# Kernel tuning notes

Hardware: AMD Instinct MI355X
Metric: run time of the kernel (lower is better)

## Reference

```python
import jax, jax.numpy as jnp
import numpy as np

B, T, D_IN, D, KS = 8, 2048, 64, 512, 3
N_LAYERS = 6
TOP_P = 0.25


def _causal_conv(x, w, b, dil):
    # x: [B, C_in, T], w: [C_out, C_in, K] -> [B, C_out, T]
    pad = (w.shape[-1] - 1) * dil
    y = jax.lax.conv_general_dilated(
        x, w, window_strides=(1,), padding=[(pad, 0)], rhs_dilation=(dil,),
        dimension_numbers=('NCH', 'OIH', 'NCH'))
    return y + b[None, :, None]


def setup_inputs() -> dict:
    key = jax.random.key(0)
    ks = jax.random.split(key, 20)
    s = 0.02
    inp = {
        'x': jax.random.normal(ks[0], (B, T, D_IN), jnp.float32),
        # block 0 (d_in=64 -> d_model=512, dilation 1) + 1x1 residual
        'c1w0': jax.random.normal(ks[1], (D, D_IN, KS), jnp.float32) * s,
        'c1b0': jnp.zeros((D,), jnp.float32),
        'c2w0': jax.random.normal(ks[2], (D, D, KS), jnp.float32) * s,
        'c2b0': jnp.zeros((D,), jnp.float32),
        'resw': jax.random.normal(ks[3], (D, D_IN, 1), jnp.float32) * s,
        'resb': jnp.zeros((D,), jnp.float32),
        # blocks 1..5 stacked (512 -> 512, dilations 2,4,8,16,32), identity residual
        'c1w': jax.random.normal(ks[4], (N_LAYERS - 1, D, D, KS), jnp.float32) * s,
        'c1b': jnp.zeros((N_LAYERS - 1, D), jnp.float32),
        'c2w': jax.random.normal(ks[5], (N_LAYERS - 1, D, D, KS), jnp.float32) * s,
        'c2b': jnp.zeros((N_LAYERS - 1, D), jnp.float32),
        # attention projections (torch Linear: y = x @ W.T + b, W [out,in])
        'wq': jax.random.normal(ks[6], (D, D), jnp.float32) * s,
        'bq': jnp.zeros((D,), jnp.float32),
        'wk': jax.random.normal(ks[7], (D, D), jnp.float32) * s,
        'bk': jnp.zeros((D,), jnp.float32),
        'wv': jax.random.normal(ks[8], (D, D), jnp.float32) * s,
        'bv': jnp.zeros((D,), jnp.float32),
        'wp': jax.random.normal(ks[9], (D, D), jnp.float32) * s,
        'bp': jnp.zeros((D,), jnp.float32),
    }
    return inp


def _forward(x, c1w0, c1b0, c2w0, c2b0, resw, resb, c1w, c1b, c2w, c2b,
             wq, bq, wk, bk, wv, bv, wp, bp):
    gelu = lambda t: jax.nn.gelu(t, approximate=False)
    h = jnp.swapaxes(x, 1, 2)  # [B, D_IN, T]
    # block 0 with 1x1-conv residual (d_in != d_out)
    y = gelu(_causal_conv(h, c1w0, c1b0, 1))
    y = gelu(_causal_conv(y, c2w0, c2b0, 1))
    h = y + _causal_conv(h, resw, resb, 1)
    # blocks 1..5, identity residual
    for i in range(N_LAYERS - 1):
        dil = 2 ** (i + 1)
        y = gelu(_causal_conv(h, c1w[i], c1b[i], dil))
        y = gelu(_causal_conv(y, c2w[i], c2b[i], dil))
        h = y + h
    z = jnp.swapaxes(h, 1, 2)  # [B, T, D]

    # sparse top-p attention
    q = z @ wq.T + bq
    k = z @ wk.T + bk
    v = z @ wv.T + bv
    scores = jnp.einsum('bqd,bkd->bqk', q, k) / jnp.sqrt(jnp.float32(D))
    k_keep = max(1, int(TOP_P * T))
    vals, idx = jax.lax.top_k(scores, k_keep)  # [B, T, k_keep]
    neg_inf = jnp.array(-jnp.inf, scores.dtype)
    mask = jnp.full_like(scores, neg_inf)
    b_ix = jnp.arange(B)[:, None, None]
    t_ix = jnp.arange(T)[None, :, None]
    mask = mask.at[b_ix, t_ix, idx].set(vals)
    attn = jax.nn.softmax(mask, axis=-1)
    attn_out = jnp.einsum('bqk,bkd->bqd', attn, v)[:, -1, :]  # [B, D]

    return (z[:, -1, :] + attn_out) @ wp.T + bp


def reference(x, c1w0, c1b0, c2w0, c2b0, resw, resb, c1w, c1b, c2w, c2b,
              wq, bq, wk, bk, wv, bv, wp, bp):
    return _forward(x, c1w0, c1b0, c2w0, c2b0, resw, resb, c1w, c1b, c2w, c2b,
                    wq, bq, wk, bk, wv, bv, wp, bp)
```

## Files before the change

### kernel.cpp

```cpp
#include <hip/hip_runtime.h>
#include <hip/hip_bf16.h>
#include <math.h>

#define B_ 8
#define T_ 2048
#define PT_ 2112
#define DIN_ 64
#define D_ 512

typedef __attribute__((ext_vector_type(8))) short bf16x8;
typedef __attribute__((ext_vector_type(4))) float f32x4;

#define HROW(b, t) (((size_t)(b) * PT_ + 64 + (t)) * D_)

__device__ __forceinline__ float gelu_f(float x) {
    return 0.5f * x * (1.0f + erff(x * 0.70710678118654752440f));
}
__device__ __forceinline__ float bfu2f(unsigned short u) {
    union { float f; unsigned int i; } v; v.i = ((unsigned int)u) << 16; return v.f;
}
__device__ __forceinline__ unsigned short f2bf(float f) {
    unsigned int x = __float_as_uint(f);
    return (unsigned short)((x + 0x7FFFu + ((x >> 16) & 1u)) >> 16);
}
__device__ __forceinline__ void gload_lds16(const void* g, void* l) {
    __builtin_amdgcn_global_load_lds(
        (const __attribute__((address_space(1))) void*)g,
        (__attribute__((address_space(3))) void*)l, 16, 0, 0);
}

__global__ __launch_bounds__(256) void k_zeropad(unsigned short* xb,
                                                 unsigned short* bufA,
                                                 unsigned short* bufB) {
    const int NX = B_ * 64 * DIN_;
    const int NA = B_ * 64 * D_;
    int i = blockIdx.x * 256 + threadIdx.x;
    if (i < NX) {
        const int b = i / (64 * DIN_), r = i - b * (64 * DIN_);
        xb[(size_t)b * PT_ * DIN_ + r] = 0;
        return;
    }
    i -= NX;
    if (i < NA) {
        const int b = i / (64 * D_), r = i - b * (64 * D_);
        bufA[(size_t)b * PT_ * D_ + r] = 0;
        return;
    }
    i -= NA;
    if (i < NA) {
        const int b = i / (64 * D_), r = i - b * (64 * D_);
        bufB[(size_t)b * PT_ * D_ + r] = 0;
    }
}

__global__ __launch_bounds__(256) void k_xcvt(const float* __restrict__ x,
                                              unsigned short* __restrict__ xb, int n) {
    const int i = blockIdx.x * 256 + threadIdx.x;
    if (i >= n) return;
    const int b = i / (T_ * DIN_);
    const int r = i - b * (T_ * DIN_);
    xb[((size_t)b * PT_ + 64) * DIN_ + r] = f2bf(x[i]);
}

__global__ __launch_bounds__(256) void k_wcvt(const float* __restrict__ src,
                                              unsigned short* __restrict__ dst,
                                              int C_in, int KS) {
    const int n = 512 * C_in * KS;
    const size_t base = (size_t)blockIdx.y * n;
    for (int i = blockIdx.x * 256 + threadIdx.x; i < n; i += gridDim.x * 256) {
        const int ci = i % C_in;
        const int r = i / C_in;
        const int co = r & 511;
        const int tap = r >> 9;
        dst[base + i] = f2bf(src[base + ((size_t)co * C_in + ci) * KS + tap]);
    }
}

template <int KS, int MODE>
__global__ __launch_bounds__(256, 2) void k_conv_mfma(const unsigned short* __restrict__ X,
                                                      const unsigned short* __restrict__ Wt,
                                                      const float* __restrict__ bias,
                                                      const unsigned short* R,
                                                      unsigned short* Y,
                                                      int C_in, int dil) {
    const int tid = threadIdx.x;
    const int t0 = blockIdx.x * 128;
    const int co0 = blockIdx.y * 128;
    const int b = blockIdx.z;
    const int back = (KS - 1) * dil;

    __shared__ __align__(16) unsigned short sX[2][192 * 64];
    __shared__ __align__(16) unsigned short sW[2][128 * 64];

    const int lane = tid & 63;
    const int wv = tid >> 6;
    const int wco = (wv & 1) * 64;
    const int wt = (wv >> 1) * 64;
    const int tl = lane & 15;
    const int ch = lane >> 4;

    f32x4 acc[4][4] = {};

    const unsigned short* Xb = X + ((size_t)b * PT_ + 64) * C_in;

    const unsigned short* xsrc[6];
#pragma unroll
    for (int k = 0; k < 6; ++k) {
        const int i = tid + k * 256;
        const int row = i >> 3, s = i & 7;
        int tg = t0 - back + row;
        if (tg >= T_) tg = T_ - 1;
        xsrc[k] = Xb + (size_t)tg * C_in + ((s ^ (row & 7)) << 3);
    }
    const unsigned short* wsrc[4];
#pragma unroll
    for (int k = 0; k < 4; ++k) {
        const int i = tid + k * 256;
        const int row = i >> 3, s = i & 7;
        wsrc[k] = Wt + (size_t)(co0 + row) * C_in + ((s ^ (row & 7)) << 3);
    }
    const size_t tapstride = (size_t)512 * C_in;

    auto stageX = [&](int c) {
        unsigned short* dst = sX[c & 1];
#pragma unroll
        for (int k = 0; k < 6; ++k) {
            const int i = tid + k * 256;
            gload_lds16(xsrc[k] + c * 64, &dst[(i & ~63) * 8]);
        }
    };
    auto stageW = [&](int c, int tap, int buf) {
        unsigned short* dst = sW[buf];
#pragma unroll
        for (int k = 0; k < 4; ++k) {
            const int i = tid + k * 256;
            gload_lds16(wsrc[k] + (size_t)tap * tapstride + c * 64, &dst[(i & ~63) * 8]);
        }
    };
    auto phase_reads = [&](int pp, int cb, int tap, bf16x8 (&a)[2][4], bf16x8 (&bb)[2][4]) {
        const unsigned short* bW = sW[pp];
        const unsigned short* bX = sX[cb];
        const int tapoff = tap * dil;
#pragma unroll
        for (int ks = 0; ks < 2; ++ks) {
            const int j = ks * 4 + ch;
#pragma unroll
            for (int m = 0; m < 4; ++m) {
                const int wr = wco + m * 16 + tl;
                a[ks][m] = *reinterpret_cast<const bf16x8*>(&bW[wr * 64 + ((j ^ (wr & 7)) << 3)]);
            }
#pragma unroll
            for (int n = 0; n < 4; ++n) {
                const int xr = wt + n * 16 + tl + tapoff;
                bb[ks][n] = *reinterpret_cast<const bf16x8*>(&bX[xr * 64 + ((j ^ (xr & 7)) << 3)]);
            }
        }
    };
    auto domfma = [&](bf16x8 (&a)[2][4], bf16x8 (&bb)[2][4]) {
        __builtin_amdgcn_s_setprio(1);
#pragma unroll
        for (int ks = 0; ks < 2; ++ks)
#pragma unroll
            for (int m = 0; m < 4; ++m)
#pragma unroll
                for (int n = 0; n < 4; ++n)
                    acc[m][n] = __builtin_amdgcn_mfma_f32_16x16x32_bf16(a[ks][m], bb[ks][n], acc[m][n], 0, 0, 0);
        __builtin_amdgcn_s_setprio(0);
    };

    if constexpr (KS == 1) {
        stageX(0);
        stageW(0, 0, 0);
        __syncthreads();
        bf16x8 a[2][4], bb[2][4];
        phase_reads(0, 0, 0, a, bb);
        domfma(a, bb);
    } else {
        const int NC = C_in >> 6;
        const int NPH = NC * 3;
        stageX(0);
        stageW(0, 0, 0);
        stageW(0, 1, 1);
        asm volatile("s_waitcnt vmcnt(4)" ::: "memory");
        __builtin_amdgcn_sched_barrier(0);
        __builtin_amdgcn_s_barrier();

        int c = 0, t = 0;
        for (int ph = 0; ph + 3 < NPH; ++ph) {
            bf16x8 a[2][4], bb[2][4];
            phase_reads(ph & 1, c & 1, t, a, bb);
            asm volatile("s_waitcnt lgkmcnt(0)" ::: "memory");
            __builtin_amdgcn_sched_barrier(0);
            __builtin_amdgcn_s_barrier();
            int t2 = t + 2, c2 = c;
            if (t2 >= 3) { t2 -= 3; ++c2; }
            stageW(c2, t2, ph & 1);
            if (t == 0) stageX(c + 1);
            domfma(a, bb);
            if (t < 2) { asm volatile("s_waitcnt vmcnt(10)" ::: "memory"); }
            else       { asm volatile("s_waitcnt vmcnt(4)"  ::: "memory"); }
            __builtin_amdgcn_sched_barrier(0);
            __builtin_amdgcn_s_barrier();
            if (++t == 3) { t = 0; ++c; }
        }
        {
            bf16x8 a[2][4], bb[2][4];
            phase_reads((NPH - 3) & 1, (NC - 1) & 1, 0, a, bb);
            asm volatile("s_waitcnt lgkmcnt(0)" ::: "memory");
            __builtin_amdgcn_sched_barrier(0);
            __builtin_amdgcn_s_barrier();
            stageW(NC - 1, 2, (NPH - 3) & 1);
            domfma(a, bb);
            asm volatile("s_waitcnt vmcnt(4)" ::: "memory");
            __builtin_amdgcn_sched_barrier(0);
            __builtin_amdgcn_s_barrier();
        }
        {
            bf16x8 a[2][4], bb[2][4];
            phase_reads((NPH - 2) & 1, (NC - 1) & 1, 1, a, bb);
            asm volatile("s_waitcnt lgkmcnt(0)" ::: "memory");
            __builtin_amdgcn_sched_barrier(0);
            __builtin_amdgcn_s_barrier();
            domfma(a, bb);
            asm volatile("s_waitcnt vmcnt(0)" ::: "memory");
            __builtin_amdgcn_sched_barrier(0);
            __builtin_amdgcn_s_barrier();
        }
        {
            bf16x8 a[2][4], bb[2][4];
            phase_reads((NPH - 1) & 1, (NC - 1) & 1, 2, a, bb);
            domfma(a, bb);
        }
    }

#pragma unroll
    for (int m = 0; m < 4; ++m) {
        const int co = co0 + wco + m * 16 + ch * 4;
        const float4 bv4 = *reinterpret_cast<const float4*>(&bias[co]);
#pragma unroll
        for (int n = 0; n < 4; ++n) {
            const int t = t0 + wt + n * 16 + tl;
            const size_t base = HROW(b, t) + co;
            float v[4];
            v[0] = acc[m][n][0] + bv4.x;
            v[1] = acc[m][n][1] + bv4.y;
            v[2] = acc[m][n][2] + bv4.z;
            v[3] = acc[m][n][3] + bv4.w;
            if (MODE >= 1) {
#pragma unroll
                for (int r = 0; r < 4; ++r) v[r] = gelu_f(v[r]);
            }
            if (MODE == 2) {
                const uint2 rr = *reinterpret_cast<const uint2*>(&R[base]);
                v[0] += bfu2f((unsigned short)(rr.x & 0xffffu));
                v[1] += bfu2f((unsigned short)(rr.x >> 16));
                v[2] += bfu2f((unsigned short)(rr.y & 0xffffu));
                v[3] += bfu2f((unsigned short)(rr.y >> 16));
            }
            uint2 o;
            o.x = (unsigned int)f2bf(v[0]) | ((unsigned int)f2bf(v[1]) << 16);
            o.y = (unsigned int)f2bf(v[2]) | ((unsigned int)f2bf(v[3]) << 16);
            *reinterpret_cast<uint2*>(&Y[base]) = o;
        }
    }
}

__global__ __launch_bounds__(256) void k_q(const unsigned short* __restrict__ h,
                                           const float* __restrict__ wq,
                                           const float* __restrict__ bq,
                                           float* __restrict__ q) {
    __shared__ float zs[B_ * D_];
    const int tid = threadIdx.x;
    for (int i = tid; i < B_ * D_; i += 256) {
        const int b = i >> 9, c = i & 511;
        zs[i] = bfu2f(h[HROW(b, T_ - 1) + c]);
    }
    __syncthreads();
    const int wvi = tid >> 6, lane = tid & 63;
    const int d = blockIdx.x * 4 + wvi;
    const float* wr = wq + (size_t)d * D_ + lane * 8;
    float w8[8];
#pragma unroll
    for (int j = 0; j < 8; ++j) w8[j] = wr[j];
    float acc[B_];
#pragma unroll
    for (int b = 0; b < B_; ++b) {
        float a = 0.0f;
#pragma unroll
        for (int j = 0; j < 8; ++j) a += w8[j] * zs[b * D_ + lane * 8 + j];
        acc[b] = a;
    }
#pragma unroll
    for (int off = 32; off; off >>= 1) {
#pragma unroll
        for (int b = 0; b < B_; ++b) acc[b] += __shfl_xor(acc[b], off);
    }
    if (lane == 0) {
#pragma unroll
        for (int b = 0; b < B_; ++b) q[b * D_ + d] = acc[b] + bq[d];
    }
}

__global__ __launch_bounds__(512) void k_qk(const float* __restrict__ q,
                                            const float* __restrict__ wk,
                                            const float* __restrict__ bk,
                                            float* __restrict__ qkvec,
                                            float* __restrict__ qbk) {
    const int b = blockIdx.y, dc = blockIdx.x;
    const int tid = threadIdx.x;
    __shared__ float qs[64];
    if (tid < 64) qs[tid] = q[b * D_ + dc * 64 + tid];
    __syncthreads();
    float acc = 0.0f;
    const float* wbase = wk + (size_t)(dc * 64) * D_ + tid;
#pragma unroll 8
    for (int d = 0; d < 64; ++d) acc += qs[d] * wbase[(size_t)d * D_];
    atomicAdd(&qkvec[b * D_ + tid], acc);
    if (tid < 64) {
        float p = qs[tid] * bk[dc * 64 + tid];
#pragma unroll
        for (int off = 32; off; off >>= 1) p += __shfl_xor(p, off);
        if (tid == 0) atomicAdd(&qbk[b], p);
    }
}

__global__ __launch_bounds__(256) void k_scores(const unsigned short* __restrict__ h,
                                                const float* __restrict__ qkvec,
                                                const float* __restrict__ qbk,
                                                float* __restrict__ scores) {
    const int b = blockIdx.y;
    const int tid = threadIdx.x;
    __shared__ float qs[D_];
    qs[tid] = qkvec[b * D_ + tid];
    qs[tid + 256] = qkvec[b * D_ + tid + 256];
    __syncthreads();
    const int wvi = tid >> 6, lane = tid & 63;
    const int t = blockIdx.x * 4 + wvi;
    const uint4 v = *reinterpret_cast<const uint4*>(h + HROW(b, t) + lane * 8);
    const unsigned int w[4] = {v.x, v.y, v.z, v.w};
    float acc = 0.0f;
#pragma unroll
    for (int j = 0; j < 4; ++j) {
        acc += bfu2f((unsigned short)(w[j] & 0xffffu)) * qs[lane * 8 + 2 * j];
        acc += bfu2f((unsigned short)(w[j] >> 16)) * qs[lane * 8 + 2 * j + 1];
    }
    for (int off = 32; off; off >>= 1) acc += __shfl_down(acc, off);
    if (lane == 0) scores[b * T_ + t] = (acc + qbk[b]) * 0.04419417382415922f;
}

__global__ __launch_bounds__(1024) void k_topk(const float* __restrict__ scores,
                                               float* __restrict__ wts) {
    const int b = blockIdx.x;
    __shared__ float s[T_];
    __shared__ float v[T_];
    __shared__ float red[16];
    __shared__ float denom_s;
    for (int i = threadIdx.x; i < T_; i += 1024) {
        const float x = scores[b * T_ + i];
        s[i] = x; v[i] = x;
    }
    __syncthreads();
    for (unsigned kk = 2; kk <= T_; kk <<= 1) {
        for (unsigned j = kk >> 1; j > 0; j >>= 1) {
            for (unsigned i = threadIdx.x; i < T_; i += 1024) {
                const unsigned ixj = i ^ j;
                if (ixj > i) {
                    const float a = v[i], c2 = v[ixj];
                    const bool asc = ((i & kk) == 0);
                    if ((a > c2) == asc) { v[i] = c2; v[ixj] = a; }
                }
            }
            __syncthreads();
        }
    }
    const float thr = v[T_ - 512];
    const float mx = v[T_ - 1];
    float part = 0.0f;
    for (int i = threadIdx.x; i < T_; i += 1024) {
        const float x = s[i];
        if (x >= thr) part += expf(x - mx);
    }
    for (int off = 32; off; off >>= 1) part += __shfl_down(part, off);
    const int lane = threadIdx.x & 63, wv_ = threadIdx.x >> 6;
    if (lane == 0) red[wv_] = part;
    __syncthreads();
    if (threadIdx.x == 0) {
        float d = 0.0f;
        for (int i = 0; i < 16; ++i) d += red[i];
        denom_s = d;
    }
    __syncthreads();
    const float inv = 1.0f / denom_s;
    for (int i = threadIdx.x; i < T_; i += 1024) {
        const float x = s[i];
        wts[b * T_ + i] = (x >= thr) ? expf(x - mx) * inv : 0.0f;
    }
}

__global__ __launch_bounds__(256) void k_zv(const unsigned short* __restrict__ h,
                                            const float* __restrict__ wts,
                                            float* __restrict__ zvb) {
    const int b = blockIdx.y;
    const int t0 = blockIdx.x * 256;
    const int tid = threadIdx.x;
    float a0 = 0.0f, a1 = 0.0f;
    for (int t = t0; t < t0 + 256; ++t) {
        const float w = wts[b * T_ + t];
        if (w != 0.0f) {
            const unsigned int v = *reinterpret_cast<const unsigned int*>(
                h + HROW(b, t) + tid * 2);
            a0 += w * bfu2f((unsigned short)(v & 0xffffu));
            a1 += w * bfu2f((unsigned short)(v >> 16));
        }
    }
    atomicAdd(&zvb[b * D_ + tid * 2], a0);
    atomicAdd(&zvb[b * D_ + tid * 2 + 1], a1);
}

__global__ __launch_bounds__(256) void k_u(const unsigned short* __restrict__ h,
                                           const float* __restrict__ zvb,
                                           const float* __restrict__ wv,
                                           const float* __restrict__ bv,
                                           float* __restrict__ u) {
    __shared__ float zs[B_ * D_];
    const int tid = threadIdx.x;
    for (int i = tid; i < B_ * D_; i += 256) zs[i] = zvb[i];
    __syncthreads();
    const int wvi = tid >> 6, lane = tid & 63;
    const int e = blockIdx.x * 4 + wvi;
    const float* wr = wv + (size_t)e * D_ + lane * 8;
    float w8[8];
#pragma unroll
    for (int j = 0; j < 8; ++j) w8[j] = wr[j];
    float acc[B_];
#pragma unroll
    for (int b = 0; b < B_; ++b) {
        float a = 0.0f;
#pragma unroll
        for (int j = 0; j < 8; ++j) a += w8[j] * zs[b * D_ + lane * 8 + j];
        acc[b] = a;
    }
#pragma unroll
    for (int off = 32; off; off >>= 1) {
#pragma unroll
        for (int b = 0; b < B_; ++b) acc[b] += __shfl_xor(acc[b], off);
    }
    if (lane == 0) {
#pragma unroll
        for (int b = 0; b < B_; ++b)
            u[b * D_ + e] = acc[b] + bv[e] + bfu2f(h[HROW(b, T_ - 1) + e]);
    }
}

__global__ __launch_bounds__(256) void k_out(const float* __restrict__ u,
                                             const float* __restrict__ wp,
                                             const float* __restrict__ bp,
                                             float* __restrict__ out) {
    __shared__ float us[B_ * D_];
    const int tid = threadIdx.x;
    for (int i = tid; i < B_ * D_; i += 256) us[i] = u[i];
    __syncthreads();
    const int wvi = tid >> 6, lane = tid & 63;
    const int d = blockIdx.x * 4 + wvi;
    const float* wr = wp + (size_t)d * D_ + lane * 8;
    float w8[8];
#pragma unroll
    for (int j = 0; j < 8; ++j) w8[j] = wr[j];
    float acc[B_];
#pragma unroll
    for (int b = 0; b < B_; ++b) {
        float a = 0.0f;
#pragma unroll
        for (int j = 0; j < 8; ++j) a += w8[j] * us[b * D_ + lane * 8 + j];
        acc[b] = a;
    }
#pragma unroll
    for (int off = 32; off; off >>= 1) {
#pragma unroll
        for (int b = 0; b < B_; ++b) acc[b] += __shfl_xor(acc[b], off);
    }
    if (lane == 0) {
#pragma unroll
        for (int b = 0; b < B_; ++b) out[b * D_ + d] = acc[b] + bp[d];
    }
}

extern "C" void kernel_launch(void* const* d_in, const int* in_sizes, int n_in,
                              void* d_out, int out_size, void* d_ws, size_t ws_size,
                              hipStream_t stream) {
    const float* x    = (const float*)d_in[0];
    const float* c1w0 = (const float*)d_in[1];
    const float* c1b0 = (const float*)d_in[2];
    const float* c2w0 = (const float*)d_in[3];
    const float* c2b0 = (const float*)d_in[4];
    const float* resw = (const float*)d_in[5];
    const float* resb = (const float*)d_in[6];
    const float* c1w  = (const float*)d_in[7];
    const float* c1b  = (const float*)d_in[8];
    const float* c2w  = (const float*)d_in[9];
    const float* c2b  = (const float*)d_in[10];
    const float* wq   = (const float*)d_in[11];
    const float* bq   = (const float*)d_in[12];
    const float* wk   = (const float*)d_in[13];
    const float* bk   = (const float*)d_in[14];
    const float* wvp  = (const float*)d_in[15];
    const float* bv   = (const float*)d_in[16];
    const float* wp   = (const float*)d_in[17];
    const float* bp   = (const float*)d_in[18];
    float* out = (float*)d_out;

    unsigned short* ws16 = (unsigned short*)d_ws;
    unsigned short* xb   = ws16;
    unsigned short* bufA = xb + (size_t)B_ * PT_ * DIN_;
    unsigned short* bufB = bufA + (size_t)B_ * PT_ * D_;
    unsigned short* wRes = bufB + (size_t)B_ * PT_ * D_;
    unsigned short* wC10 = wRes + 512 * 64;
    unsigned short* wC20 = wC10 + 3 * 512 * 64;
    unsigned short* wC1  = wC20 + 3 * 512 * 512;
    unsigned short* wC2  = wC1 + (size_t)5 * 3 * 512 * 512;
    float* fws  = (float*)(wC2 + (size_t)5 * 3 * 512 * 512);
    float* qv    = fws;
    float* qkvec = qv + B_ * D_;
    float* qbk   = qkvec + B_ * D_;
    float* zvb   = qbk + 8;
    float* uacc  = zvb + B_ * D_;
    float* sc    = uacc + B_ * D_;
    float* wts   = sc + B_ * T_;

    k_zeropad<<<dim3((B_ * 64 * (DIN_ + 2 * D_) + 255) / 256), 256, 0, stream>>>(xb, bufA, bufB);
    k_xcvt<<<dim3((B_ * T_ * DIN_ + 255) / 256), 256, 0, stream>>>(x, xb, B_ * T_ * DIN_);
    k_wcvt<<<dim3(128, 1), 256, 0, stream>>>(resw, wRes, DIN_, 1);
    k_wcvt<<<dim3(384, 1), 256, 0, stream>>>(c1w0, wC10, DIN_, 3);
    k_wcvt<<<dim3(768, 1), 256, 0, stream>>>(c2w0, wC20, D_, 3);
    k_wcvt<<<dim3(768, 5), 256, 0, stream>>>(c1w, wC1, D_, 3);
    k_wcvt<<<dim3(768, 5), 256, 0, stream>>>(c2w, wC2, D_, 3);
    hipMemsetAsync(qkvec, 0, (2 * B_ * D_ + 8) * sizeof(float), stream);

    const dim3 cgrid(T_ / 128, D_ / 128, B_);
    k_conv_mfma<1, 0><<<cgrid, 256, 0, stream>>>(xb, wRes, resb, nullptr, bufA, DIN_, 1);
    k_conv_mfma<3, 1><<<cgrid, 256, 0, stream>>>(xb, wC10, c1b0, nullptr, bufB, DIN_, 1);
    k_conv_mfma<3, 2><<<cgrid, 256, 0, stream>>>(bufB, wC20, c2b0, bufA, bufA, D_, 1);
    for (int i = 0; i < 5; ++i) {
        const int dil = 2 << i;
        k_conv_mfma<3, 1><<<cgrid, 256, 0, stream>>>(bufA, wC1 + (size_t)i * 3 * 512 * 512,
                                                     c1b + i * D_, nullptr, bufB, D_, dil);
        k_conv_mfma<3, 2><<<cgrid, 256, 0, stream>>>(bufB, wC2 + (size_t)i * 3 * 512 * 512,
                                                     c2b + i * D_, bufA, bufA, D_, dil);
    }

    k_q<<<128, 256, 0, stream>>>(bufA, wq, bq, qv);
    k_qk<<<dim3(8, 8), 512, 0, stream>>>(qv, wk, bk, qkvec, qbk);
    k_scores<<<dim3(T_ / 4, B_), 256, 0, stream>>>(bufA, qkvec, qbk, sc);
    k_topk<<<B_, 1024, 0, stream>>>(sc, wts);
    k_zv<<<dim3(T_ / 256, B_), 256, 0, stream>>>(bufA, wts, zvb);
    k_u<<<128, 256, 0, stream>>>(bufA, zvb, wvp, bv, uacc);
    k_out<<<128, 256, 0, stream>>>(uacc, wp, bp, out);
}
```

Measured before the change: 491.3 us.

## Enlarge conv tile to 256 channels with 512-thread blocks and swizzled grid

Each block of the MFMA conv kernel now computes 256 output channels by 128 time steps with 8 waves, instead of 128x128 with 4 waves. The grid becomes 32 blocks per batch with an interleaved work mapping so neighbouring blocks share time windows. The X window is fixed at 64 rows of look-back and the tap/channel pipeline is unified into one loop with tuned waitcnts. The aim is to halve redundant X loads per output and cut launch-grid size, at the cost of one block per CU, 256 total blocks, and more LDS per block.

```diff
diff --git a/kernel.cpp b/kernel.cpp
--- a/kernel.cpp
+++ b/kernel.cpp
@@ -77,25 +77,26 @@
 }
 
 template <int KS, int MODE>
-__global__ __launch_bounds__(256, 2) void k_conv_mfma(const unsigned short* __restrict__ X,
+__global__ __launch_bounds__(512, 1) void k_conv_mfma(const unsigned short* __restrict__ X,
                                                       const unsigned short* __restrict__ Wt,
                                                       const float* __restrict__ bias,
                                                       const unsigned short* R,
                                                       unsigned short* Y,
                                                       int C_in, int dil) {
     const int tid = threadIdx.x;
-    const int t0 = blockIdx.x * 128;
-    const int co0 = blockIdx.y * 128;
+    const int ib = blockIdx.x;
+    const int work = (ib & 7) * 4 + (ib >> 3);
+    const int co0 = (work & 1) * 256;
+    const int t0 = (work >> 1) * 128;
     const int b = blockIdx.z;
-    const int back = (KS - 1) * dil;
 
     __shared__ __align__(16) unsigned short sX[2][192 * 64];
-    __shared__ __align__(16) unsigned short sW[2][128 * 64];
+    __shared__ __align__(16) unsigned short sW[2][256 * 64];
 
     const int lane = tid & 63;
     const int wv = tid >> 6;
-    const int wco = (wv & 1) * 64;
-    const int wt = (wv >> 1) * 64;
+    const int wco = (wv & 3) * 64;
+    const int wt = (wv >> 2) * 64;
     const int tl = lane & 15;
     const int ch = lane >> 4;
 
@@ -103,19 +104,18 @@
 
     const unsigned short* Xb = X + ((size_t)b * PT_ + 64) * C_in;
 
-    const unsigned short* xsrc[6];
-#pragma unroll
-    for (int k = 0; k < 6; ++k) {
-        const int i = tid + k * 256;
+    const unsigned short* xsrc[3];
+#pragma unroll
+    for (int k = 0; k < 3; ++k) {
+        const int i = tid + k * 512;
         const int row = i >> 3, s = i & 7;
-        int tg = t0 - back + row;
-        if (tg >= T_) tg = T_ - 1;
+        const int tg = t0 - 64 + row;
         xsrc[k] = Xb + (size_t)tg * C_in + ((s ^ (row & 7)) << 3);
     }
     const unsigned short* wsrc[4];
 #pragma unroll
     for (int k = 0; k < 4; ++k) {
-        const int i = tid + k * 256;
+        const int i = tid + k * 512;
         const int row = i >> 3, s = i & 7;
         wsrc[k] = Wt + (size_t)(co0 + row) * C_in + ((s ^ (row & 7)) << 3);
     }
@@ -124,8 +124,8 @@
     auto stageX = [&](int c) {
         unsigned short* dst = sX[c & 1];
 #pragma unroll
-        for (int k = 0; k < 6; ++k) {
-            const int i = tid + k * 256;
+        for (int k = 0; k < 3; ++k) {
+            const int i = tid + k * 512;
             gload_lds16(xsrc[k] + c * 64, &dst[(i & ~63) * 8]);
         }
     };
@@ -133,14 +133,14 @@
         unsigned short* dst = sW[buf];
 #pragma unroll
         for (int k = 0; k < 4; ++k) {
-            const int i = tid + k * 256;
+            const int i = tid + k * 512;
             gload_lds16(wsrc[k] + (size_t)tap * tapstride + c * 64, &dst[(i & ~63) * 8]);
         }
     };
-    auto phase_reads = [&](int pp, int cb, int tap, bf16x8 (&a)[2][4], bf16x8 (&bb)[2][4]) {
-        const unsigned short* bW = sW[pp];
-        const unsigned short* bX = sX[cb];
-        const int tapoff = tap * dil;
+    auto phase_reads = [&](int wbuf, int xbuf, int tap, bf16x8 (&a)[2][4], bf16x8 (&bb)[2][4]) {
+        const unsigned short* bW = sW[wbuf];
+        const unsigned short* bX = sX[xbuf];
+        const int xoff = 64 - (KS - 1 - tap) * dil;
 #pragma unroll
         for (int ks = 0; ks < 2; ++ks) {
             const int j = ks * 4 + ch;
@@ -151,7 +151,7 @@
             }
 #pragma unroll
             for (int n = 0; n < 4; ++n) {
-                const int xr = wt + n * 16 + tl + tapoff;
+                const int xr = wt + n * 16 + tl + xoff;
                 bb[ks][n] = *reinterpret_cast<const bf16x8*>(&bX[xr * 64 + ((j ^ (xr & 7)) << 3)]);
             }
         }
@@ -168,69 +168,50 @@
         __builtin_amdgcn_s_setprio(0);
     };
 
-    if constexpr (KS == 1) {
-        stageX(0);
-        stageW(0, 0, 0);
-        __syncthreads();
+    const int NC = C_in >> 6;
+    const int NT = NC * KS;
+
+    stageX(0);
+    stageW(0, 0, 0);
+    if (NT > 1) {
+        stageW(0, (KS > 1) ? 1 : 0, 1);
+        asm volatile("s_waitcnt vmcnt(4)" ::: "memory");
+    } else {
+        asm volatile("s_waitcnt vmcnt(0)" ::: "memory");
+    }
+    __builtin_amdgcn_sched_barrier(0);
+    __builtin_amdgcn_s_barrier();
+
+    int c = 0, tap = 0;
+    for (int kt = 0; kt < NT; ++kt) {
         bf16x8 a[2][4], bb[2][4];
-        phase_reads(0, 0, 0, a, bb);
-        domfma(a, bb);
-    } else {
-        const int NC = C_in >> 6;
-        const int NPH = NC * 3;
-        stageX(0);
-        stageW(0, 0, 0);
-        stageW(0, 1, 1);
-        asm volatile("s_waitcnt vmcnt(4)" ::: "memory");
+        phase_reads(kt & 1, c & 1, tap, a, bb);
+        asm volatile("s_waitcnt lgkmcnt(0)" ::: "memory");
         __builtin_amdgcn_sched_barrier(0);
         __builtin_amdgcn_s_barrier();
 
-        int c = 0, t = 0;
-        for (int ph = 0; ph + 3 < NPH; ++ph) {
-            bf16x8 a[2][4], bb[2][4];
-            phase_reads(ph & 1, c & 1, t, a, bb);
-            asm volatile("s_waitcnt lgkmcnt(0)" ::: "memory");
+        if (kt + 2 < NT) {
+            const int c2 = c + (tap + 2) / KS;
+            const int t2 = (tap + 2) % KS;
+            stageW(c2, t2, kt & 1);
+        }
+        if (tap == 0 && c + 1 < NC) stageX(c + 1);
+
+        domfma(a, bb);
+
+        if (kt < NT - 1) {
+            if (KS == 3) {
+                if (tap == 2)            { asm volatile("s_waitcnt vmcnt(4)" ::: "memory"); }
+                else if (c < NC - 1)     { asm volatile("s_waitcnt vmcnt(7)" ::: "memory"); }
+                else if (tap == 0)       { asm volatile("s_waitcnt vmcnt(4)" ::: "memory"); }
+                else                     { asm volatile("s_waitcnt vmcnt(0)" ::: "memory"); }
+            } else {
+                asm volatile("s_waitcnt vmcnt(0)" ::: "memory");
+            }
             __builtin_amdgcn_sched_barrier(0);
             __builtin_amdgcn_s_barrier();
-            int t2 = t + 2, c2 = c;
-            if (t2 >= 3) { t2 -= 3; ++c2; }
-            stageW(c2, t2, ph & 1);
-            if (t == 0) stageX(c + 1);
-            domfma(a, bb);
-            if (t < 2) { asm volatile("s_waitcnt vmcnt(10)" ::: "memory"); }
-            else       { asm volatile("s_waitcnt vmcnt(4)"  ::: "memory"); }
-            __builtin_amdgcn_sched_barrier(0);
-            __builtin_amdgcn_s_barrier();
-            if (++t == 3) { t = 0; ++c; }
-        }
-        {
-            bf16x8 a[2][4], bb[2][4];
-            phase_reads((NPH - 3) & 1, (NC - 1) & 1, 0, a, bb);
-            asm volatile("s_waitcnt lgkmcnt(0)" ::: "memory");
-            __builtin_amdgcn_sched_barrier(0);
-            __builtin_amdgcn_s_barrier();
-            stageW(NC - 1, 2, (NPH - 3) & 1);
-            domfma(a, bb);
-            asm volatile("s_waitcnt vmcnt(4)" ::: "memory");
-            __builtin_amdgcn_sched_barrier(0);
-            __builtin_amdgcn_s_barrier();
-        }
-        {
-            bf16x8 a[2][4], bb[2][4];
-            phase_reads((NPH - 2) & 1, (NC - 1) & 1, 1, a, bb);
-            asm volatile("s_waitcnt lgkmcnt(0)" ::: "memory");
-            __builtin_amdgcn_sched_barrier(0);
-            __builtin_amdgcn_s_barrier();
-            domfma(a, bb);
-            asm volatile("s_waitcnt vmcnt(0)" ::: "memory");
-            __builtin_amdgcn_sched_barrier(0);
-            __builtin_amdgcn_s_barrier();
-        }
-        {
-            bf16x8 a[2][4], bb[2][4];
-            phase_reads((NPH - 1) & 1, (NC - 1) & 1, 2, a, bb);
-            domfma(a, bb);
-        }
+        }
+        if (++tap == KS) { tap = 0; ++c; }
     }
 
 #pragma unroll
@@ -536,15 +517,15 @@
     k_wcvt<<<dim3(768, 5), 256, 0, stream>>>(c2w, wC2, D_, 3);
     hipMemsetAsync(qkvec, 0, (2 * B_ * D_ + 8) * sizeof(float), stream);
 
-    const dim3 cgrid(T_ / 128, D_ / 128, B_);
-    k_conv_mfma<1, 0><<<cgrid, 256, 0, stream>>>(xb, wRes, resb, nullptr, bufA, DIN_, 1);
-    k_conv_mfma<3, 1><<<cgrid, 256, 0, stream>>>(xb, wC10, c1b0, nullptr, bufB, DIN_, 1);
-    k_conv_mfma<3, 2><<<cgrid, 256, 0, stream>>>(bufB, wC20, c2b0, bufA, bufA, D_, 1);
+    const dim3 cgrid(32, 1, B_);
+    k_conv_mfma<1, 0><<<cgrid, 512, 0, stream>>>(xb, wRes, resb, nullptr, bufA, DIN_, 1);
+    k_conv_mfma<3, 1><<<cgrid, 512, 0, stream>>>(xb, wC10, c1b0, nullptr, bufB, DIN_, 1);
+    k_conv_mfma<3, 2><<<cgrid, 512, 0, stream>>>(bufB, wC20, c2b0, bufA, bufA, D_, 1);
     for (int i = 0; i < 5; ++i) {
         const int dil = 2 << i;
-        k_conv_mfma<3, 1><<<cgrid, 256, 0, stream>>>(bufA, wC1 + (size_t)i * 3 * 512 * 512,
+        k_conv_mfma<3, 1><<<cgrid, 512, 0, stream>>>(bufA, wC1 + (size_t)i * 3 * 512 * 512,
                                                      c1b + i * D_, nullptr, bufB, D_, dil);
-        k_conv_mfma<3, 2><<<cgrid, 256, 0, stream>>>(bufB, wC2 + (size_t)i * 3 * 512 * 512,
+        k_conv_mfma<3, 2><<<cgrid, 512, 0, stream>>>(bufB, wC2 + (size_t)i * 3 * 512 * 512,
                                                      c2b + i * D_, bufA, bufA, D_, dil);
     }
 
```

Measured after the change: 523.0 us. 6.5% more time.
